# Performance work log

Measured on AMD Instinct MI355X. Metric: run time of the kernel, lower is better.

## Reference

```python
import jax, jax.numpy as jnp
import numpy as np

N = 50000        # nodes
E = 250000       # edges (avg degree 5)
D = 32           # embed_dim
N_LAYERS = 3


def _uniform(key, shape, fan_in):
    s = 1.0 / np.sqrt(fan_in)
    return jax.random.uniform(key, shape, jnp.float32, -s, s)


def setup_inputs() -> dict:
    key = jax.random.key(0)
    ks = jax.random.split(key, 10)
    x = jax.random.normal(ks[0], (N, 1), jnp.float32)
    edge_index = jax.random.randint(ks[1], (2, E), 0, N, dtype=jnp.int64)
    edge_attribute = jax.random.normal(ks[2], (E, 1), jnp.float32)
    # Linear weights stored as [in, out] (i.e. torch weight transposed)
    node_W = _uniform(ks[3], (1, D), 1)
    node_b = _uniform(ks[4], (D,), 1)
    l1_W = _uniform(ks[5], (1, D * D), 1)
    l1_b = _uniform(ks[6], (D * D,), 1)
    root = _uniform(ks[7], (D, D), D)      # NNConv root weight
    conv_b = _uniform(ks[8], (D,), D)      # NNConv bias
    return {
        "x": x, "edge_index": edge_index, "edge_attribute": edge_attribute,
        "i": 2, "dummy": 0,
        "node_W": node_W, "node_b": node_b,
        "l1_W": l1_W, "l1_b": l1_b,
        "root": root, "conv_b": conv_b,
    }


def reference(x, edge_index, edge_attribute, i, dummy, node_W, node_b,
              l1_W, l1_b, root, conv_b):
    n_encode_layers = min(i + 1, N_LAYERS)
    src, dst = edge_index[0], edge_index[1]

    # node embedding: [N,1] -> [N,D]
    h = x @ node_W + node_b

    # edge-conditioned weight matrices, shared by every layer: [E, D, D]
    We = (edge_attribute @ l1_W + l1_b).reshape(E, D, D)

    # mean-aggregation denominator (in-degree, clamped; isolated nodes -> 0 msg)
    cnt = jax.ops.segment_sum(jnp.ones((E,), h.dtype), dst, num_segments=N)
    cnt = jnp.maximum(cnt, 1.0)[:, None]

    for _ in range(n_encode_layers):
        h = jax.nn.relu(h)
        # gather source features, per-edge matmul: msg_e = x_src[e] @ We[e]
        msg = jnp.einsum('ei,eio->eo', h[src], We)
        aggr = jax.ops.segment_sum(msg, dst, num_segments=N) / cnt
        h = aggr + h @ root + conv_b
    return h
```

## Files before the change

### kernel.cpp

```cpp
#include <hip/hip_runtime.h>
#include <hip/hip_bf16.h>

#define N_NODES 50000
#define N_EDGES 250000
#define DIM 32
#define BLK 256
#define CAP 16
#define SPILL_MAX 4096
#define EDGE_NB 977
#define WCONV_NB 13
#define LAYER_NB 1563
#define POISON 0xAAAAAAAAu

typedef __attribute__((ext_vector_type(8))) short short8;
typedef __attribute__((ext_vector_type(4))) float f32x4;

__device__ __forceinline__ float ldf(const void* p, int i, int isf32) {
    return isf32 ? ((const float*)p)[i]
                 : __bfloat162float(((const __hip_bfloat16*)p)[i]);
}
__device__ __forceinline__ float b2f(unsigned int u16) {
    return __uint_as_float(u16 << 16);
}
__device__ __forceinline__ int ldi(const int* ei, int i, int i64) {
    return i64 ? ei[2 * i] : ei[i];
}
__device__ __forceinline__ int clamp_idx(int v) {
    v = v < 0 ? 0 : v;
    return v >= N_NODES ? N_NODES - 1 : v;
}
__device__ __forceinline__ bool half_is_big(const void* p, int k) {
    unsigned short h = ((const unsigned short*)p)[k];
    float v = __uint_as_float(((unsigned int)h) << 16);
    return !(fabsf(v) <= 50.0f);
}
__device__ __forceinline__ unsigned short bf16bits(float v) {
    __hip_bfloat16 b = __float2bfloat16(v);
    return __builtin_bit_cast(unsigned short, b);
}
__device__ __forceinline__ unsigned int pack2(float lo, float hi) {
    return ((unsigned int)bf16bits(hi) << 16) | (unsigned int)bf16bits(lo);
}

__global__ __launch_bounds__(BLK) void prep_kernel(
    const int* __restrict__ ei, const void* __restrict__ ea,
    const void* __restrict__ lW, const void* __restrict__ lb,
    const void* __restrict__ rt, const void* __restrict__ cb,
    int* __restrict__ cntI, int2* __restrict__ packed,
    int* __restrict__ spill_cnt, int4* __restrict__ spill,
    float* __restrict__ wCB, unsigned short* __restrict__ wfrag)
{
    __shared__ int sdet;
    int tid = threadIdx.x;
    int b = blockIdx.x;
    if (tid == 0) sdet = 0;
    __syncthreads();

    if (b < EDGE_NB) {
        if (tid < 64) {
            if (ei[2 * tid + 1] != 0) atomicOr(&sdet, 2);
        } else if (tid < 192) {
            if (half_is_big(ea, tid - 64)) atomicOr(&sdet, 1);
        }
        __syncthreads();
        int f_ea = sdet & 1, i64 = ((sdet & 2) == 0);
        int e = b * BLK + tid;
        if (e < N_EDGES) {
            int s = clamp_idx(ldi(ei, e, i64));
            int d = clamp_idx(ldi(ei, N_EDGES + e, i64));
            float a = ldf(ea, e, f_ea);
            unsigned k = (unsigned)atomicAdd(&cntI[d], 1) - POISON;
            if (k < CAP) {
                packed[d * CAP + (int)k] = make_int2(s, __float_as_int(a));
            } else {
                unsigned sp = (unsigned)atomicAdd(spill_cnt, 1) - POISON;
                if (sp < SPILL_MAX)
                    spill[sp] = make_int4(d, s, __float_as_int(a), 0);
            }
        }
        return;
    }

    if (tid < 64)       { if (half_is_big(lW, tid) || half_is_big(lW, tid + 64)) atomicOr(&sdet, 1); }
    else if (tid < 128) { int k = tid - 64;  if (half_is_big(lb, k) || half_is_big(lb, k + 64)) atomicOr(&sdet, 2); }
    else if (tid < 192) { int k = tid - 128; if (half_is_big(rt, k) || half_is_big(rt, k + 64)) atomicOr(&sdet, 4); }
    else if (tid < 224) { if (half_is_big(cb, tid - 192)) atomicOr(&sdet, 8); }
    __syncthreads();
    int fW = sdet & 1, fB = sdet & 2, fR = sdet & 4, fC = sdet & 8;
    int g = (int)(b - EDGE_NB) * BLK + tid;
    if (g < 3072) {
        int f = g >> 9, rem = g & 511;
        int ln = rem >> 3, j = rem & 7;
        int t = f >> 1, nh = f & 1;
        int k = t * 32 + (ln >> 4) * 8 + j;
        int n = nh * 16 + (ln & 15);
        float v;
        if (k < 32)      v = ldf(lW, k * 32 + n, fW);
        else if (k < 64) v = ldf(lb, (k - 32) * 32 + n, fB);
        else             v = ldf(rt, (k - 64) * 32 + n, fR);
        wfrag[g] = bf16bits(v);
    } else if (g < 3104) {
        wCB[g - 3072] = ldf(cb, g - 3072, fC);
    }
}

__global__ __launch_bounds__(512) void layer_kernel(
    const int2* __restrict__ packed, const int* __restrict__ cntI,
    const int* __restrict__ spill_cnt, const int4* __restrict__ spill,
    const void* __restrict__ x, const void* __restrict__ nW,
    const void* __restrict__ nb,
    const unsigned int* __restrict__ hin,
    const float* __restrict__ wCB,
    const unsigned short* __restrict__ wfrag,
    void* __restrict__ outb, int mode0, int last)
{
    __shared__ __align__(16) unsigned int sAu32[32 * 48];
    __shared__ int sdet;
    int tid = threadIdx.x;
    int wv = tid >> 6;
    int lane = tid & 63;
    int q = lane >> 4;
    int l16 = lane & 15;
    int nbase = blockIdx.x * 32;
    int n0 = nbase + wv * 4;

    float nW2lo = 0.0f, nW2hi = 0.0f, nb2lo = 0.0f, nb2hi = 0.0f;
    int f_x = 0;
    if (mode0) {
        if (tid == 0) sdet = 0;
        __syncthreads();
        if (tid < 128) {
            if (half_is_big(x, tid)) atomicOr(&sdet, 4);
        } else if (tid < 160) {
            if (half_is_big(nW, tid - 128)) atomicOr(&sdet, 8);
        } else if (tid < 192) {
            if (half_is_big(nb, tid - 160)) atomicOr(&sdet, 16);
        }
        __syncthreads();
        f_x = sdet & 4;
        nW2lo = ldf(nW, 2 * l16,     sdet & 8);
        nW2hi = ldf(nW, 2 * l16 + 1, sdet & 8);
        nb2lo = ldf(nb, 2 * l16,     sdet & 16);
        nb2hi = ldf(nb, 2 * l16 + 1, sdet & 16);
    }

    int4 c[4];
    #pragma unroll
    for (int j = 0; j < 4; ++j)
        c[j] = *(const int4*)(packed + (n0 + j) * CAP + 2 * q);

    int deg[4];
    if (n0 + 3 < N_NODES) {
        int4 d4 = *(const int4*)(cntI + n0);
        deg[0] = (int)((unsigned)d4.x - POISON);
        deg[1] = (int)((unsigned)d4.y - POISON);
        deg[2] = (int)((unsigned)d4.z - POISON);
        deg[3] = (int)((unsigned)d4.w - POISON);
    } else {
        #pragma unroll
        for (int j = 0; j < 4; ++j) {
            int n = n0 + j;
            deg[j] = (n < N_NODES) ? (int)((unsigned)cntI[n] - POISON) : 0;
        }
    }

    float hslo, hshi;
    {
        int ns = clamp_idx(n0 + q);
        if (mode0) {
            float xs = ldf(x, ns, f_x);
            hslo = fmaf(xs, nW2lo, nb2lo); hslo = hslo > 0.0f ? hslo : 0.0f;
            hshi = fmaf(xs, nW2hi, nb2hi); hshi = hshi > 0.0f ? hshi : 0.0f;
        } else {
            unsigned int u = hin[ns * 16 + l16];
            hslo = b2f(u & 0xffffu);
            hshi = b2f(u >> 16);
        }
    }

    float plo[4] = {0,0,0,0}, phi[4] = {0,0,0,0};
    float qlo[4] = {0,0,0,0}, qhi[4] = {0,0,0,0};
    #pragma unroll
    for (int j = 0; j < 4; ++j) {
        int s0 = clamp_idx(c[j].x), s1 = clamp_idx(c[j].z);
        float a0 = __int_as_float(c[j].y), a1 = __int_as_float(c[j].w);
        float h0lo, h0hi, h1lo, h1hi;
        if (mode0) {
            float xs0 = ldf(x, s0, f_x), xs1 = ldf(x, s1, f_x);
            h0lo = fmaf(xs0, nW2lo, nb2lo); h0lo = h0lo > 0.0f ? h0lo : 0.0f;
            h0hi = fmaf(xs0, nW2hi, nb2hi); h0hi = h0hi > 0.0f ? h0hi : 0.0f;
            h1lo = fmaf(xs1, nW2lo, nb2lo); h1lo = h1lo > 0.0f ? h1lo : 0.0f;
            h1hi = fmaf(xs1, nW2hi, nb2hi); h1hi = h1hi > 0.0f ? h1hi : 0.0f;
        } else {
            unsigned int u0 = hin[s0 * 16 + l16];
            unsigned int u1 = hin[s1 * 16 + l16];
            h0lo = b2f(u0 & 0xffffu); h0hi = b2f(u0 >> 16);
            h1lo = b2f(u1 & 0xffffu); h1hi = b2f(u1 >> 16);
        }
        bool v0 = (2 * q)     < deg[j];
        bool v1 = (2 * q + 1) < deg[j];
        float a0m = v0 ? a0 : 0.0f, a1m = v1 ? a1 : 0.0f;
        float h0lom = v0 ? h0lo : 0.0f, h0him = v0 ? h0hi : 0.0f;
        float h1lom = v1 ? h1lo : 0.0f, h1him = v1 ? h1hi : 0.0f;
        plo[j] = fmaf(a0m, h0lom, plo[j]); plo[j] = fmaf(a1m, h1lom, plo[j]);
        phi[j] = fmaf(a0m, h0him, phi[j]); phi[j] = fmaf(a1m, h1him, phi[j]);
        qlo[j] += h0lom + h1lom;
        qhi[j] += h0him + h1him;
    }
    #pragma unroll
    for (int j = 0; j < 4; ++j) {
        if (deg[j] > 8) {
            int4 c2 = *(const int4*)(packed + (n0 + j) * CAP + 8 + 2 * q);
            int dgc = deg[j] < CAP ? deg[j] : CAP;
            int s0 = clamp_idx(c2.x), s1 = clamp_idx(c2.z);
            float a0 = __int_as_float(c2.y), a1 = __int_as_float(c2.w);
            float h0lo, h0hi, h1lo, h1hi;
            if (mode0) {
                float xs0 = ldf(x, s0, f_x), xs1 = ldf(x, s1, f_x);
                h0lo = fmaf(xs0, nW2lo, nb2lo); h0lo = h0lo > 0.0f ? h0lo : 0.0f;
                h0hi = fmaf(xs0, nW2hi, nb2hi); h0hi = h0hi > 0.0f ? h0hi : 0.0f;
                h1lo = fmaf(xs1, nW2lo, nb2lo); h1lo = h1lo > 0.0f ? h1lo : 0.0f;
                h1hi = fmaf(xs1, nW2hi, nb2hi); h1hi = h1hi > 0.0f ? h1hi : 0.0f;
            } else {
                unsigned int u0 = hin[s0 * 16 + l16];
                unsigned int u1 = hin[s1 * 16 + l16];
                h0lo = b2f(u0 & 0xffffu); h0hi = b2f(u0 >> 16);
                h1lo = b2f(u1 & 0xffffu); h1hi = b2f(u1 >> 16);
            }
            bool v0 = (8 + 2 * q)     < dgc;
            bool v1 = (8 + 2 * q + 1) < dgc;
            float a0m = v0 ? a0 : 0.0f, a1m = v1 ? a1 : 0.0f;
            float h0lom = v0 ? h0lo : 0.0f, h0him = v0 ? h0hi : 0.0f;
            float h1lom = v1 ? h1lo : 0.0f, h1him = v1 ? h1hi : 0.0f;
            plo[j] = fmaf(a0m, h0lom, plo[j]); plo[j] = fmaf(a1m, h1lom, plo[j]);
            phi[j] = fmaf(a0m, h0him, phi[j]); phi[j] = fmaf(a1m, h1him, phi[j]);
            qlo[j] += h0lom + h1lom;
            qhi[j] += h0him + h1him;
        }
    }
    unsigned spt = (unsigned)(*spill_cnt) - POISON;
    if (spt != 0) {
        if (spt > SPILL_MAX) spt = SPILL_MAX;
        #pragma unroll
        for (int j = 0; j < 4; ++j) {
            if (deg[j] > CAP) {
                for (unsigned t = (unsigned)q; t < spt; t += 4) {
                    int4 sp = spill[t];
                    if (sp.x == n0 + j) {
                        float hvlo, hvhi;
                        if (mode0) {
                            float xs = ldf(x, clamp_idx(sp.y), f_x);
                            hvlo = fmaf(xs, nW2lo, nb2lo); hvlo = hvlo > 0.0f ? hvlo : 0.0f;
                            hvhi = fmaf(xs, nW2hi, nb2hi); hvhi = hvhi > 0.0f ? hvhi : 0.0f;
                        } else {
                            unsigned int u = hin[clamp_idx(sp.y) * 16 + l16];
                            hvlo = b2f(u & 0xffffu); hvhi = b2f(u >> 16);
                        }
                        float a = __int_as_float(sp.z);
                        plo[j] = fmaf(a, hvlo, plo[j]);
                        phi[j] = fmaf(a, hvhi, phi[j]);
                        qlo[j] += hvlo; qhi[j] += hvhi;
                    }
                }
            }
        }
    }
    #pragma unroll
    for (int j = 0; j < 4; ++j) {
        plo[j] += __shfl_xor(plo[j], 16); plo[j] += __shfl_xor(plo[j], 32);
        phi[j] += __shfl_xor(phi[j], 16); phi[j] += __shfl_xor(phi[j], 32);
        qlo[j] += __shfl_xor(qlo[j], 16); qlo[j] += __shfl_xor(qlo[j], 32);
        qhi[j] += __shfl_xor(qhi[j], 16); qhi[j] += __shfl_xor(qhi[j], 32);
    }
    #pragma unroll
    for (int j = 0; j < 4; ++j) {
        float ic = 1.0f / (deg[j] < 1 ? 1.0f : (float)deg[j]);
        if (q == 0)
            sAu32[(wv * 4 + j) * 48 + l16]      = pack2(plo[j] * ic, phi[j] * ic);
        else if (q == 1)
            sAu32[(wv * 4 + j) * 48 + 16 + l16] = pack2(qlo[j] * ic, qhi[j] * ic);
    }
    sAu32[(wv * 4 + q) * 48 + 32 + l16] = pack2(hslo, hshi);
    __syncthreads();

    if (wv < 4) {
        const unsigned short* sAu = (const unsigned short*)sAu32;
        int rg = wv & 1, nh = wv >> 1;
        short8 bfr[3];
        #pragma unroll
        for (int t = 0; t < 3; ++t)
            bfr[t] = *(const short8*)(wfrag + ((t * 2 + nh) * 64 + lane) * 8);
        f32x4 acc = {0.0f, 0.0f, 0.0f, 0.0f};
        #pragma unroll
        for (int t = 0; t < 3; ++t) {
            short8 afr = *(const short8*)(sAu + (rg * 16 + (lane & 15)) * 96
                                          + t * 32 + (lane >> 4) * 8);
            acc = __builtin_amdgcn_mfma_f32_16x16x32_bf16(afr, bfr[t], acc, 0, 0, 0);
        }
        float cbl = wCB[nh * 16 + (lane & 15)];
        #pragma unroll
        for (int r = 0; r < 4; ++r) {
            int row = rg * 16 + (lane >> 4) * 4 + r;
            int n = nbase + row;
            if (n < N_NODES) {
                float v = acc[r] + cbl;
                int col = nh * 16 + (lane & 15);
                if (!last) {
                    v = v > 0.0f ? v : 0.0f;
                    ((unsigned short*)outb)[n * DIM + col] = bf16bits(v);
                } else {
                    ((float*)outb)[n * DIM + col] = v;
                }
            }
        }
    }
}

extern "C" void kernel_launch(void* const* d_in, const int* in_sizes, int n_in,
                              void* d_out, int out_size, void* d_ws, size_t ws_size,
                              hipStream_t stream) {
    const void* p[16];
    int np_ = 0;
    for (int i = 0; i < n_in && np_ < 16; ++i)
        if (in_sizes[i] != 1) p[np_++] = d_in[i];

    const void* x      = p[0];
    const int*  ei     = (const int*)p[1];
    const void* ea     = p[2];
    const void* node_W = p[3];
    const void* node_b = p[4];
    const void* l1_W   = p[5];
    const void* l1_b   = p[6];
    const void* root   = p[7];
    const void* conv_b = p[8];
    float* out = (float*)d_out;

    const int ND = N_NODES * DIM;
    char* ws = (char*)d_ws;
    int2*  packed    = (int2*)ws;
    unsigned int* hr1 = (unsigned int*)(packed + N_NODES * CAP);
    unsigned int* hr2 = hr1 + N_NODES * 16;
    float* wCB       = (float*)(hr2 + N_NODES * 16);
    unsigned short* wfrag = (unsigned short*)(wCB + 32);
    int*   cntI      = (int*)(wfrag + 3072);
    int*   spill_cnt = cntI + N_NODES;
    int4*  spill     = (int4*)(spill_cnt + 4);

    prep_kernel<<<EDGE_NB + WCONV_NB, BLK, 0, stream>>>(
        ei, ea, l1_W, l1_b, root, conv_b,
        cntI, packed, spill_cnt, spill, wCB, wfrag);

    layer_kernel<<<LAYER_NB, 512, 0, stream>>>(packed, cntI, spill_cnt, spill,
        x, node_W, node_b, hr2 , wCB, wfrag, hr1, 1, 0);
    layer_kernel<<<LAYER_NB, 512, 0, stream>>>(packed, cntI, spill_cnt, spill,
        x, node_W, node_b, hr1, wCB, wfrag, hr2, 0, 0);
    layer_kernel<<<LAYER_NB, 512, 0, stream>>>(packed, cntI, spill_cnt, spill,
        x, node_W, node_b, hr2, wCB, wfrag, out, 0, 1);
}
```

Baseline: 136.5 us.

## Fuse three layer launches into one persistent cooperative kernel with grid sync

Replaces the three per-layer kernel launches with a single cooperative persistent kernel. It loops over layers with a grid-wide barrier between them and strides node tiles across a fixed grid of 256 or 512 blocks. Each block loads the MFMA weight fragments and node-embedding parameters once and prefetches the next tile's adjacency while working on the current one. This targets launch gaps and per-block setup, at the cost of grid-sync overhead and possibly lower parallelism. The old three-kernel path remains as a fallback if the cooperative launch fails.

```diff
diff --git a/kernel.cpp b/kernel.cpp
--- a/kernel.cpp
+++ b/kernel.cpp
@@ -1,5 +1,8 @@
 #include <hip/hip_runtime.h>
 #include <hip/hip_bf16.h>
+#include <hip/hip_cooperative_groups.h>
+
+namespace cg = cooperative_groups;
 
 #define N_NODES 50000
 #define N_EDGES 250000
@@ -101,6 +104,267 @@
         wfrag[g] = bf16bits(v);
     } else if (g < 3104) {
         wCB[g - 3072] = ldf(cb, g - 3072, fC);
+    }
+}
+
+__global__ __launch_bounds__(512, 4) void layers_fused(
+    const int2* __restrict__ packed, const int* __restrict__ cntI,
+    const int* __restrict__ spill_cnt, const int4* __restrict__ spill,
+    const void* __restrict__ x, const void* __restrict__ nW,
+    const void* __restrict__ nb,
+    unsigned int* __restrict__ hr1, unsigned int* __restrict__ hr2,
+    const float* __restrict__ wCB, const unsigned short* __restrict__ wfrag,
+    float* __restrict__ out)
+{
+    __shared__ __align__(16) unsigned int sAu32[32 * 48];
+    __shared__ int sdet;
+    cg::grid_group gg = cg::this_grid();
+    int tid = threadIdx.x;
+    int b = (int)blockIdx.x;
+    int gsz = (int)gridDim.x;
+    int wv = tid >> 6;
+    int lane = tid & 63;
+    int q = lane >> 4;
+    int l16 = lane & 15;
+
+    if (tid == 0) sdet = 0;
+    __syncthreads();
+    if (tid < 128)      { if (half_is_big(x, tid)) atomicOr(&sdet, 4); }
+    else if (tid < 160) { if (half_is_big(nW, tid - 128)) atomicOr(&sdet, 8); }
+    else if (tid < 192) { if (half_is_big(nb, tid - 160)) atomicOr(&sdet, 16); }
+    __syncthreads();
+    int f_x = sdet & 4;
+    float nW2lo = ldf(nW, 2 * l16,     sdet & 8);
+    float nW2hi = ldf(nW, 2 * l16 + 1, sdet & 8);
+    float nb2lo = ldf(nb, 2 * l16,     sdet & 16);
+    float nb2hi = ldf(nb, 2 * l16 + 1, sdet & 16);
+
+    short8 bfr[3];
+    {
+        int nh = (wv >> 1) & 1;
+        #pragma unroll
+        for (int t = 0; t < 3; ++t)
+            bfr[t] = *(const short8*)(wfrag + ((t * 2 + nh) * 64 + lane) * 8);
+    }
+    float cbl = wCB[((wv >> 1) & 1) * 16 + (lane & 15)];
+
+    unsigned spt0 = (unsigned)(*spill_cnt) - POISON;
+    if (spt0 > SPILL_MAX) spt0 = SPILL_MAX;
+
+    #pragma unroll 1
+    for (int l = 0; l < 3; ++l) {
+        const unsigned int* hin = (l == 1) ? hr1 : hr2;
+        void* outb = (l == 0) ? (void*)hr1 : (l == 1) ? (void*)hr2 : (void*)out;
+        int mode0 = (l == 0);
+        int last = (l == 2);
+
+        int4 cc[4];
+        int4 dd;
+        {
+            int n0p = b * 32 + wv * 4;
+            #pragma unroll
+            for (int j = 0; j < 4; ++j)
+                cc[j] = *(const int4*)(packed + (n0p + j) * CAP + 2 * q);
+            dd = *(const int4*)(cntI + n0p);
+        }
+
+        #pragma unroll 1
+        for (int unit = b; unit < LAYER_NB; unit += gsz) {
+            int nbase = unit * 32;
+            int n0 = nbase + wv * 4;
+
+            int deg[4];
+            {
+                int dr[4] = {dd.x, dd.y, dd.z, dd.w};
+                #pragma unroll
+                for (int j = 0; j < 4; ++j)
+                    deg[j] = (n0 + j < N_NODES)
+                           ? (int)((unsigned)dr[j] - POISON) : 0;
+            }
+            int s0i[4], s1i[4];
+            float a0f[4], a1f[4];
+            #pragma unroll
+            for (int j = 0; j < 4; ++j) {
+                s0i[j] = clamp_idx(cc[j].x); a0f[j] = __int_as_float(cc[j].y);
+                s1i[j] = clamp_idx(cc[j].z); a1f[j] = __int_as_float(cc[j].w);
+            }
+
+            int nxt = unit + gsz;
+            int4 cn[4];
+            int4 dn;
+            if (nxt < LAYER_NB) {
+                int n0n = nxt * 32 + wv * 4;
+                #pragma unroll
+                for (int j = 0; j < 4; ++j)
+                    cn[j] = *(const int4*)(packed + (n0n + j) * CAP + 2 * q);
+                dn = *(const int4*)(cntI + n0n);
+            }
+
+            float h0lo[4], h0hi[4], h1lo[4], h1hi[4];
+            float hslo, hshi;
+            if (mode0) {
+                float xs0[4], xs1[4];
+                #pragma unroll
+                for (int j = 0; j < 4; ++j) {
+                    xs0[j] = ldf(x, s0i[j], f_x);
+                    xs1[j] = ldf(x, s1i[j], f_x);
+                }
+                float xss = ldf(x, clamp_idx(n0 + q), f_x);
+                #pragma unroll
+                for (int j = 0; j < 4; ++j) {
+                    float t0 = fmaf(xs0[j], nW2lo, nb2lo); h0lo[j] = t0 > 0.0f ? t0 : 0.0f;
+                    float t1 = fmaf(xs0[j], nW2hi, nb2hi); h0hi[j] = t1 > 0.0f ? t1 : 0.0f;
+                    float t2 = fmaf(xs1[j], nW2lo, nb2lo); h1lo[j] = t2 > 0.0f ? t2 : 0.0f;
+                    float t3 = fmaf(xs1[j], nW2hi, nb2hi); h1hi[j] = t3 > 0.0f ? t3 : 0.0f;
+                }
+                float ts0 = fmaf(xss, nW2lo, nb2lo); hslo = ts0 > 0.0f ? ts0 : 0.0f;
+                float ts1 = fmaf(xss, nW2hi, nb2hi); hshi = ts1 > 0.0f ? ts1 : 0.0f;
+            } else {
+                unsigned int u0[4], u1[4];
+                #pragma unroll
+                for (int j = 0; j < 4; ++j) {
+                    u0[j] = hin[s0i[j] * 16 + l16];
+                    u1[j] = hin[s1i[j] * 16 + l16];
+                }
+                unsigned int us = hin[clamp_idx(n0 + q) * 16 + l16];
+                #pragma unroll
+                for (int j = 0; j < 4; ++j) {
+                    h0lo[j] = b2f(u0[j] & 0xffffu); h0hi[j] = b2f(u0[j] >> 16);
+                    h1lo[j] = b2f(u1[j] & 0xffffu); h1hi[j] = b2f(u1[j] >> 16);
+                }
+                hslo = b2f(us & 0xffffu); hshi = b2f(us >> 16);
+            }
+
+            float plo[4] = {0,0,0,0}, phi[4] = {0,0,0,0};
+            float qlo[4] = {0,0,0,0}, qhi[4] = {0,0,0,0};
+            #pragma unroll
+            for (int j = 0; j < 4; ++j) {
+                bool v0 = (2 * q)     < deg[j];
+                bool v1 = (2 * q + 1) < deg[j];
+                float a0m = v0 ? a0f[j] : 0.0f, a1m = v1 ? a1f[j] : 0.0f;
+                float h0lom = v0 ? h0lo[j] : 0.0f, h0him = v0 ? h0hi[j] : 0.0f;
+                float h1lom = v1 ? h1lo[j] : 0.0f, h1him = v1 ? h1hi[j] : 0.0f;
+                plo[j] = fmaf(a0m, h0lom, plo[j]); plo[j] = fmaf(a1m, h1lom, plo[j]);
+                phi[j] = fmaf(a0m, h0him, phi[j]); phi[j] = fmaf(a1m, h1him, phi[j]);
+                qlo[j] += h0lom + h1lom;
+                qhi[j] += h0him + h1him;
+            }
+            #pragma unroll
+            for (int j = 0; j < 4; ++j) {
+                if (deg[j] > 8) {
+                    int4 c2 = *(const int4*)(packed + (n0 + j) * CAP + 8 + 2 * q);
+                    int dgc = deg[j] < CAP ? deg[j] : CAP;
+                    int s0 = clamp_idx(c2.x), s1 = clamp_idx(c2.z);
+                    float a0 = __int_as_float(c2.y), a1 = __int_as_float(c2.w);
+                    float t0lo, t0hi, t1lo, t1hi;
+                    if (mode0) {
+                        float xs0 = ldf(x, s0, f_x), xs1 = ldf(x, s1, f_x);
+                        t0lo = fmaf(xs0, nW2lo, nb2lo); t0lo = t0lo > 0.0f ? t0lo : 0.0f;
+                        t0hi = fmaf(xs0, nW2hi, nb2hi); t0hi = t0hi > 0.0f ? t0hi : 0.0f;
+                        t1lo = fmaf(xs1, nW2lo, nb2lo); t1lo = t1lo > 0.0f ? t1lo : 0.0f;
+                        t1hi = fmaf(xs1, nW2hi, nb2hi); t1hi = t1hi > 0.0f ? t1hi : 0.0f;
+                    } else {
+                        unsigned int w0 = hin[s0 * 16 + l16];
+                        unsigned int w1 = hin[s1 * 16 + l16];
+                        t0lo = b2f(w0 & 0xffffu); t0hi = b2f(w0 >> 16);
+                        t1lo = b2f(w1 & 0xffffu); t1hi = b2f(w1 >> 16);
+                    }
+                    bool v0 = (8 + 2 * q)     < dgc;
+                    bool v1 = (8 + 2 * q + 1) < dgc;
+                    float a0m = v0 ? a0 : 0.0f, a1m = v1 ? a1 : 0.0f;
+                    float g0lo = v0 ? t0lo : 0.0f, g0hi = v0 ? t0hi : 0.0f;
+                    float g1lo = v1 ? t1lo : 0.0f, g1hi = v1 ? t1hi : 0.0f;
+                    plo[j] = fmaf(a0m, g0lo, plo[j]); plo[j] = fmaf(a1m, g1lo, plo[j]);
+                    phi[j] = fmaf(a0m, g0hi, phi[j]); phi[j] = fmaf(a1m, g1hi, phi[j]);
+                    qlo[j] += g0lo + g1lo;
+                    qhi[j] += g0hi + g1hi;
+                }
+            }
+            if (spt0 != 0) {
+                #pragma unroll
+                for (int j = 0; j < 4; ++j) {
+                    if (deg[j] > CAP) {
+                        for (unsigned t = (unsigned)q; t < spt0; t += 4) {
+                            int4 sp = spill[t];
+                            if (sp.x == n0 + j) {
+                                float hvlo, hvhi;
+                                if (mode0) {
+                                    float xs = ldf(x, clamp_idx(sp.y), f_x);
+                                    hvlo = fmaf(xs, nW2lo, nb2lo); hvlo = hvlo > 0.0f ? hvlo : 0.0f;
+                                    hvhi = fmaf(xs, nW2hi, nb2hi); hvhi = hvhi > 0.0f ? hvhi : 0.0f;
+                                } else {
+                                    unsigned int u = hin[clamp_idx(sp.y) * 16 + l16];
+                                    hvlo = b2f(u & 0xffffu); hvhi = b2f(u >> 16);
+                                }
+                                float a = __int_as_float(sp.z);
+                                plo[j] = fmaf(a, hvlo, plo[j]);
+                                phi[j] = fmaf(a, hvhi, phi[j]);
+                                qlo[j] += hvlo; qhi[j] += hvhi;
+                            }
+                        }
+                    }
+                }
+            }
+            #pragma unroll
+            for (int j = 0; j < 4; ++j) {
+                plo[j] += __shfl_xor(plo[j], 16); plo[j] += __shfl_xor(plo[j], 32);
+                phi[j] += __shfl_xor(phi[j], 16); phi[j] += __shfl_xor(phi[j], 32);
+                qlo[j] += __shfl_xor(qlo[j], 16); qlo[j] += __shfl_xor(qlo[j], 32);
+                qhi[j] += __shfl_xor(qhi[j], 16); qhi[j] += __shfl_xor(qhi[j], 32);
+            }
+
+            __builtin_amdgcn_s_barrier();
+            asm volatile("" ::: "memory");
+
+            #pragma unroll
+            for (int j = 0; j < 4; ++j) {
+                float ic = 1.0f / (deg[j] < 1 ? 1.0f : (float)deg[j]);
+                if (q == 0)
+                    sAu32[(wv * 4 + j) * 48 + l16]      = pack2(plo[j] * ic, phi[j] * ic);
+                else if (q == 1)
+                    sAu32[(wv * 4 + j) * 48 + 16 + l16] = pack2(qlo[j] * ic, qhi[j] * ic);
+            }
+            sAu32[(wv * 4 + q) * 48 + 32 + l16] = pack2(hslo, hshi);
+            asm volatile("s_waitcnt lgkmcnt(0)" ::: "memory");
+            __builtin_amdgcn_s_barrier();
+            asm volatile("" ::: "memory");
+
+            if (wv < 4) {
+                const unsigned short* sAu = (const unsigned short*)sAu32;
+                int rg = wv & 1, nh = wv >> 1;
+                f32x4 acc = {0.0f, 0.0f, 0.0f, 0.0f};
+                #pragma unroll
+                for (int t = 0; t < 3; ++t) {
+                    short8 afr = *(const short8*)(sAu
+                        + (rg * 16 + (lane & 15)) * 96
+                        + t * 32 + (lane >> 4) * 8);
+                    acc = __builtin_amdgcn_mfma_f32_16x16x32_bf16(
+                              afr, bfr[t], acc, 0, 0, 0);
+                }
+                #pragma unroll
+                for (int r = 0; r < 4; ++r) {
+                    int row = rg * 16 + (lane >> 4) * 4 + r;
+                    int n = nbase + row;
+                    if (n < N_NODES) {
+                        float v = acc[r] + cbl;
+                        int col = nh * 16 + (lane & 15);
+                        if (!last) {
+                            v = v > 0.0f ? v : 0.0f;
+                            ((unsigned short*)outb)[n * DIM + col] = bf16bits(v);
+                        } else {
+                            ((float*)outb)[n * DIM + col] = v;
+                        }
+                    }
+                }
+            }
+
+            if (nxt < LAYER_NB) {
+                #pragma unroll
+                for (int j = 0; j < 4; ++j) cc[j] = cn[j];
+                dd = dn;
+            }
+        }
+        if (l < 2) gg.sync();
     }
 }
 
@@ -335,7 +599,6 @@
     const void* conv_b = p[8];
     float* out = (float*)d_out;
 
-    const int ND = N_NODES * DIM;
     char* ws = (char*)d_ws;
     int2*  packed    = (int2*)ws;
     unsigned int* hr1 = (unsigned int*)(packed + N_NODES * CAP);
@@ -350,10 +613,26 @@
         ei, ea, l1_W, l1_b, root, conv_b,
         cntI, packed, spill_cnt, spill, wCB, wfrag);
 
-    layer_kernel<<<LAYER_NB, 512, 0, stream>>>(packed, cntI, spill_cnt, spill,
-        x, node_W, node_b, hr2 , wCB, wfrag, hr1, 1, 0);
-    layer_kernel<<<LAYER_NB, 512, 0, stream>>>(packed, cntI, spill_cnt, spill,
-        x, node_W, node_b, hr1, wCB, wfrag, hr2, 0, 0);
-    layer_kernel<<<LAYER_NB, 512, 0, stream>>>(packed, cntI, spill_cnt, spill,
-        x, node_W, node_b, hr2, wCB, wfrag, out, 0, 1);
-}
+    int maxb = 0;
+    hipError_t qerr = hipOccupancyMaxActiveBlocksPerMultiprocessor(
+        &maxb, (const void*)layers_fused, 512, 0);
+    hipError_t lerr = hipErrorUnknown;
+    if (qerr == hipSuccess && maxb >= 1) {
+        int grid = (maxb >= 2) ? 512 : 256;
+        void* args[] = {
+            (void*)&packed, (void*)&cntI, (void*)&spill_cnt, (void*)&spill,
+            (void*)&x, (void*)&node_W, (void*)&node_b,
+            (void*)&hr1, (void*)&hr2, (void*)&wCB, (void*)&wfrag, (void*)&out
+        };
+        lerr = hipLaunchCooperativeKernel(
+            (const void*)layers_fused, dim3(grid), dim3(512), args, 0, stream);
+    }
+    if (lerr != hipSuccess) {
+        layer_kernel<<<LAYER_NB, 512, 0, stream>>>(packed, cntI, spill_cnt,
+            spill, x, node_W, node_b, hr2 , wCB, wfrag, hr1, 1, 0);
+        layer_kernel<<<LAYER_NB, 512, 0, stream>>>(packed, cntI, spill_cnt,
+            spill, x, node_W, node_b, hr1, wCB, wfrag, hr2, 0, 0);
+        layer_kernel<<<LAYER_NB, 512, 0, stream>>>(packed, cntI, spill_cnt,
+            spill, x, node_W, node_b, hr2, wCB, wfrag, out, 0, 1);
+    }
+}
```

New measurement: 237.8 us. 1.74x slower.
